# Performance work log

Hardware: AMD Instinct MI355X
Metric: run time of the kernel (lower is better)

The kernel has to match this reference:

```python
import jax, jax.numpy as jnp
import numpy as np

DIM = 1024
HEADS = 16
DIM_HEAD = 64
INNER = HEADS * DIM_HEAD  # 1024
SCALE = DIM_HEAD ** -0.5


def setup_inputs() -> dict:
    key = jax.random.key(0)
    k1, k2, k3, k4 = jax.random.split(key, 4)
    B, N = 2, 2048
    x = jax.random.normal(k1, (B, N, DIM), dtype=jnp.float32)
    # to_qkv: Linear(dim, 3*inner_dim, bias=False); weight stored as [out, in] in torch,
    # here as [in, out] for x @ W.
    w_qkv = jax.random.normal(k2, (DIM, 3 * INNER), dtype=jnp.float32) * (DIM ** -0.5)
    # to_out: Linear(inner_dim, dim) with bias
    w_out = jax.random.normal(k3, (INNER, DIM), dtype=jnp.float32) * (INNER ** -0.5)
    b_out = jax.random.normal(k4, (DIM,), dtype=jnp.float32) * 0.02
    return {"x": x, "w_qkv": w_qkv, "w_out": w_out, "b_out": b_out}


def reference(x, w_qkv, w_out, b_out):
    B, N, _ = x.shape
    qkv = x @ w_qkv                                  # [B, N, 3*INNER]
    q, k, v = jnp.split(qkv, 3, axis=-1)             # each [B, N, INNER]
    def to_heads(t):
        return t.reshape(B, N, HEADS, DIM_HEAD).transpose(0, 2, 1, 3)  # [B,H,N,D]
    q, k, v = to_heads(q), to_heads(k), to_heads(v)
    dots = jnp.einsum('bhnd,bhmd->bhnm', q, k) * SCALE  # [B,H,N,N]
    attn = jax.nn.softmax(dots, axis=-1)
    out = jnp.einsum('bhnm,bhmd->bhnd', attn, v)        # [B,H,N,D]
    out = out.transpose(0, 2, 1, 3).reshape(B, N, INNER)
    return out @ w_out + b_out
```

## Files before the change

kernel.cpp:

```cpp
#include <hip/hip_runtime.h>
#include <hip/hip_bf16.h>
#include <stdint.h>

#define PDIM   1024
#define HEADS  16
#define DHEAD  64
#define BATCH  2
#define SEQ    2048
#define ROWS   (BATCH*SEQ)
#define NBH    (BATCH*HEADS)

typedef __attribute__((ext_vector_type(8))) short s8v;
typedef __attribute__((ext_vector_type(4))) float f32x4;
typedef __attribute__((ext_vector_type(16))) float f32x16;
typedef unsigned short ushort_t;
typedef unsigned int   uint32;

#define QSCALE 0.18033688011112042f
#define MFIX 12.0f

__device__ __forceinline__ ushort_t f2bf(float x){
  union { float f; uint32 u; } v; v.f = x;
  uint32 r = v.u + 0x7FFFu + ((v.u >> 16) & 1u);
  return (ushort_t)(r >> 16);
}
__device__ __forceinline__ uint32 cvt_pk_bf16(float lo, float hi){
  uint32 r;
  asm("v_cvt_pk_bf16_f32 %0, %1, %2" : "=v"(r) : "v"(lo), "v"(hi));
  return r;
}

typedef const __attribute__((address_space(1))) void* gas_ptr;
typedef __attribute__((address_space(3))) void*       las_ptr;
__device__ __forceinline__ void g2l16(const void* g, void* l){
  __builtin_amdgcn_global_load_lds((gas_ptr)g, (las_ptr)l, 16, 0, 0);
}

__global__ __launch_bounds__(256) void k_prep(
    const float* __restrict__ x, const float* __restrict__ w_qkv,
    const float* __restrict__ w_out,
    ushort_t* __restrict__ Xh, ushort_t* __restrict__ Wqt_h,
    ushort_t* __restrict__ Wot_h){
  __shared__ float tile[64][65];
  const int bid = blockIdx.x;
  if (bid < 4096){
    int i = bid * 256 + threadIdx.x;
    float4 v = reinterpret_cast<const float4*>(x)[i];
    reinterpret_cast<ushort4*>(Xh)[i] =
        make_ushort4(f2bf(v.x), f2bf(v.y), f2bf(v.z), f2bf(v.w));
    return;
  }
  const float* src; ushort_t* dst; int R, C, cb, rb;
  float scl = 1.f;
  if (bid < 4864){
    int t = bid - 4096; src = w_qkv; dst = Wqt_h; R = 1024; C = 3072;
    cb = (t % 48) * 64; rb = (t / 48) * 64;
    if (cb < 1024) scl = QSCALE;
  } else {
    int t = bid - 4864; src = w_out; dst = Wot_h; R = 1024; C = 1024;
    cb = (t % 16) * 64; rb = (t / 16) * 64;
  }
  int t = threadIdx.x;
  int lw = t >> 6, lc = t & 63;
#pragma unroll
  for (int i = 0; i < 16; i++){
    int r = i * 4 + lw;
    tile[r][lc] = src[(size_t)(rb + r) * C + cb + lc];
  }
  __syncthreads();
#pragma unroll
  for (int i = 0; i < 16; i++){
    int c = i * 4 + lw;
    dst[(size_t)(cb + c) * R + rb + lc] = f2bf(tile[lc][c] * scl);
  }
}

#define GBM 128
#define GBN 128
#define GBK 64

__global__ __launch_bounds__(256, 2) void k_gemm_qkv(
    const ushort_t* __restrict__ Xh, const ushort_t* __restrict__ Wqt_h,
    ushort_t* __restrict__ Qh, ushort_t* __restrict__ Kh, ushort_t* __restrict__ Vth){
  __shared__ __align__(16) ushort_t Asm[2][GBM * GBK];
  __shared__ __align__(16) ushort_t Bsm[2][GBM * GBK];
  const int tid  = threadIdx.x;
  const int wave = tid >> 6, lane = tid & 63;
  const int mb = blockIdx.y * GBM, nb = blockIdx.x * GBN;
  const int wr = wave >> 1, wc = wave & 1;
  const int l15 = lane & 15, l4 = lane >> 4;
  const int rsub = lane >> 3;
  const int schunk = ((lane & 7) ^ rsub) * 8;
  f32x4 acc[4][4] = {};

  auto stage = [&](int buf, int kb){
    int k0 = kb * GBK;
#pragma unroll
    for (int i = 0; i < 4; i++){
      int row = (i * 4 + wave) * 8 + rsub;
      g2l16(Xh    + (size_t)(mb + row) * 1024 + k0 + schunk, &Asm[buf][(i * 4 + wave) * 512]);
      g2l16(Wqt_h + (size_t)(nb + row) * 1024 + k0 + schunk, &Bsm[buf][(i * 4 + wave) * 512]);
    }
  };

  stage(0, 0);

  for (int kb = 0; kb < 16; kb++){
    const int cur = kb & 1;
    if (kb < 15){
      stage(cur ^ 1, kb + 1);
      asm volatile("s_waitcnt vmcnt(8)" ::: "memory");
    } else {
      asm volatile("s_waitcnt vmcnt(0)" ::: "memory");
    }
    __builtin_amdgcn_s_barrier();
    __builtin_amdgcn_s_setprio(1);
#pragma unroll
    for (int ks = 0; ks < 2; ks++){
      s8v af[4], bfr[4];
#pragma unroll
      for (int f = 0; f < 4; f++){
        int ch = (((ks * 4 + l4) ^ (l15 & 7)) << 3);
        af[f]  = *reinterpret_cast<const s8v*>(&Asm[cur][(wr * 64 + f * 16 + l15) * 64 + ch]);
        bfr[f] = *reinterpret_cast<const s8v*>(&Bsm[cur][(wc * 64 + f * 16 + l15) * 64 + ch]);
      }
#pragma unroll
      for (int fr = 0; fr < 4; fr++)
#pragma unroll
        for (int fc = 0; fc < 4; fc++)
          acc[fr][fc] = __builtin_amdgcn_mfma_f32_16x16x32_bf16(af[fr], bfr[fc], acc[fr][fc], 0, 0, 0);
    }
    __builtin_amdgcn_s_setprio(0);
    __builtin_amdgcn_s_barrier();
  }

  const int pnum = nb >> 10;
#pragma unroll
  for (int fr = 0; fr < 4; fr++){
    int row  = mb + wr * 64 + fr * 16 + l4 * 4;
    int b    = row >> 11;
    int nseq = row & 2047;
#pragma unroll
    for (int fc = 0; fc < 4; fc++){
      int col = nb + wc * 64 + fc * 16 + l15;
      int rem = col & 1023;
      int h = rem >> 6, d = rem & 63;
      int bh = b * 16 + h;
      if (pnum == 0){
        size_t base = ((size_t)bh * SEQ + nseq) * 64 + d;
#pragma unroll
        for (int r = 0; r < 4; r++)
          Qh[base + (size_t)r * 64] = f2bf(acc[fr][fc][r]);
      } else if (pnum == 1){
        size_t base = ((size_t)bh * SEQ + nseq) * 64 + d;
#pragma unroll
        for (int r = 0; r < 4; r++)
          Kh[base + (size_t)r * 64] = f2bf(acc[fr][fc][r]);
      } else {
        size_t base = ((size_t)bh * 64 + d) * SEQ + nseq;
        *reinterpret_cast<ushort4*>(&Vth[base]) =
            make_ushort4(f2bf(acc[fr][fc][0]), f2bf(acc[fr][fc][1]),
                         f2bf(acc[fr][fc][2]), f2bf(acc[fr][fc][3]));
      }
    }
  }
}

__global__ __launch_bounds__(256, 2) void k_gemm_out(
    const ushort_t* __restrict__ Ah, const ushort_t* __restrict__ Bth,
    float* __restrict__ C, const float* __restrict__ bias){
  __shared__ __align__(16) ushort_t Asm[2][GBM * GBK];
  __shared__ __align__(16) ushort_t Bsm[2][GBM * GBK];
  const int tid  = threadIdx.x;
  const int wave = tid >> 6, lane = tid & 63;
  const int mb = blockIdx.y * GBM, nb = blockIdx.x * GBN;
  const int wr = wave >> 1, wc = wave & 1;
  const int l15 = lane & 15, l4 = lane >> 4;
  const int rsub = lane >> 3;
  const int schunk = ((lane & 7) ^ rsub) * 8;
  f32x4 acc[4][4] = {};

  auto stage = [&](int buf, int kb){
    int k0 = kb * GBK;
#pragma unroll
    for (int i = 0; i < 4; i++){
      int row = (i * 4 + wave) * 8 + rsub;
      g2l16(Ah  + (size_t)(mb + row) * 1024 + k0 + schunk, &Asm[buf][(i * 4 + wave) * 512]);
      g2l16(Bth + (size_t)(nb + row) * 1024 + k0 + schunk, &Bsm[buf][(i * 4 + wave) * 512]);
    }
  };

  stage(0, 0);

  for (int kb = 0; kb < 16; kb++){
    const int cur = kb & 1;
    if (kb < 15){
      stage(cur ^ 1, kb + 1);
      asm volatile("s_waitcnt vmcnt(8)" ::: "memory");
    } else {
      asm volatile("s_waitcnt vmcnt(0)" ::: "memory");
    }
    __builtin_amdgcn_s_barrier();
    __builtin_amdgcn_s_setprio(1);
#pragma unroll
    for (int ks = 0; ks < 2; ks++){
      s8v af[4], bfr[4];
#pragma unroll
      for (int f = 0; f < 4; f++){
        int ch = (((ks * 4 + l4) ^ (l15 & 7)) << 3);
        af[f]  = *reinterpret_cast<const s8v*>(&Asm[cur][(wr * 64 + f * 16 + l15) * 64 + ch]);
        bfr[f] = *reinterpret_cast<const s8v*>(&Bsm[cur][(wc * 64 + f * 16 + l15) * 64 + ch]);
      }
#pragma unroll
      for (int fr = 0; fr < 4; fr++)
#pragma unroll
        for (int fc = 0; fc < 4; fc++)
          acc[fr][fc] = __builtin_amdgcn_mfma_f32_16x16x32_bf16(af[fr], bfr[fc], acc[fr][fc], 0, 0, 0);
    }
    __builtin_amdgcn_s_setprio(0);
    __builtin_amdgcn_s_barrier();
  }
#pragma unroll
  for (int fr = 0; fr < 4; fr++){
    int row = mb + wr * 64 + fr * 16 + l4 * 4;
#pragma unroll
    for (int fc = 0; fc < 4; fc++){
      int col = nb + wc * 64 + fc * 16 + l15;
      float bv = bias[col];
#pragma unroll
      for (int r = 0; r < 4; r++)
        C[(size_t)(row + r) * 1024 + col] = acc[fr][fc][r] + bv;
    }
  }
}

__global__ __launch_bounds__(128, 4) void k_flash(
    const ushort_t* __restrict__ Qh, const ushort_t* __restrict__ Kh,
    const ushort_t* __restrict__ Vth, ushort_t* __restrict__ Ah){
  __shared__ __align__(16) ushort_t KhS[2][32 * 64];
  __shared__ __align__(16) ushort_t VhS[2][64 * 32];
  const int lid = blockIdx.x;
  const int xcd = lid & 7, g = lid >> 3;
  const int bh = xcd * 4 + (g & 3);
  const int qb = (g >> 2) * 64;
  const int tid = threadIdx.x, wave = tid >> 6, lane = tid & 63;
  const int l31 = lane & 31, hh = lane >> 5;
  const int b = bh >> 4, hd = bh & 15;
  const size_t hbase = (size_t)bh * SEQ * 64;
  const int rsub = lane >> 3;
  const int schunkK = ((lane & 7) ^ rsub) * 8;
  const int schunkV = ((lane & 3) ^ ((lane >> 2) & 3)) * 8;

  int fchK[4], fchV[2];
#pragma unroll
  for (int s = 0; s < 4; s++) fchK[s] = (((2 * s + hh) ^ (l31 & 7)) << 3);
#pragma unroll
  for (int s = 0; s < 2; s++) fchV[s] = (((2 * s + hh) ^ (l31 & 3)) << 3);
  const int fbK = l31 * 64;
  const int fbV = l31 * 32;

  s8v qf[4];
#pragma unroll
  for (int s = 0; s < 4; s++)
    qf[s] = *reinterpret_cast<const s8v*>(
        &Qh[hbase + (size_t)(qb + wave * 32 + l31) * 64 + s * 16 + hh * 8]);

  f32x16 o0 = {}, o1 = {};
  float lsum = 0.f;

  const ushort_t* kp0 = Kh + hbase + (size_t)(wave * 8 + rsub) * 64 + schunkK;
  const ushort_t* kp1 = kp0 + (size_t)16 * 64;
  const ushort_t* vp0 = Vth + ((size_t)bh * 64 + wave * 16 + (lane >> 2)) * SEQ + schunkV;
  const ushort_t* vp1 = vp0 + (size_t)32 * SEQ;

  auto stage = [&](int buf){
    g2l16(kp0, &KhS[buf][wave * 512]);        kp0 += 2048;
    g2l16(kp1, &KhS[buf][1024 + wave * 512]); kp1 += 2048;
    g2l16(vp0, &VhS[buf][wave * 512]);        vp0 += 32;
    g2l16(vp1, &VhS[buf][1024 + wave * 512]); vp1 += 32;
  };

  stage(0);

  for (int kt = 0; kt < 64; kt++){
    const int cur = kt & 1;
    if (kt < 63){
      stage(cur ^ 1);
      asm volatile("s_waitcnt vmcnt(4)" ::: "memory");
    } else {
      asm volatile("s_waitcnt vmcnt(0)" ::: "memory");
    }
    __builtin_amdgcn_s_barrier();

    f32x16 s0 = {};
    __builtin_amdgcn_s_setprio(1);
#pragma unroll
    for (int s = 0; s < 4; s++){
      s8v kf = *reinterpret_cast<const s8v*>(&KhS[cur][fbK + fchK[s]]);
      s0 = __builtin_amdgcn_mfma_f32_32x32x16_bf16(kf, qf[s], s0, 0, 0, 0);
    }
    __builtin_amdgcn_s_setprio(0);

    uint32 w[8];
#pragma unroll
    for (int t = 0; t < 8; t++){
      float pa = __builtin_amdgcn_exp2f(s0[2 * t]     - MFIX);
      float pb = __builtin_amdgcn_exp2f(s0[2 * t + 1] - MFIX);
      lsum += pa + pb;
      w[t] = cvt_pk_bf16(pa, pb);
    }

    __builtin_amdgcn_s_setprio(1);
#pragma unroll
    for (int s = 0; s < 2; s++){
      const int u = 4 * s;
      uint32 m0 = w[u],     m2 = w[u + 2];
      uint32 m1 = w[u + 1], m3 = w[u + 3];
      asm("v_permlane32_swap_b32 %0, %1" : "+v"(m0), "+v"(m2));
      asm("v_permlane32_swap_b32 %0, %1" : "+v"(m1), "+v"(m3));
      union { uint32 u4[4]; s8v v; } pf;
      pf.u4[0] = m0; pf.u4[1] = m1; pf.u4[2] = m2; pf.u4[3] = m3;
      s8v vf0 = *reinterpret_cast<const s8v*>(&VhS[cur][fbV + fchV[s]]);
      s8v vf1 = *reinterpret_cast<const s8v*>(&VhS[cur][fbV + 1024 + fchV[s]]);
      o0 = __builtin_amdgcn_mfma_f32_32x32x16_bf16(pf.v, vf0, o0, 0, 0, 0);
      o1 = __builtin_amdgcn_mfma_f32_32x32x16_bf16(pf.v, vf1, o1, 0, 0, 0);
    }
    __builtin_amdgcn_s_setprio(0);
    __builtin_amdgcn_s_barrier();
  }

  lsum += __shfl_xor(lsum, 32);
  float linv = 1.f / lsum;
#pragma unroll
  for (int r = 0; r < 16; r++){
    int q = (r & 3) + 8 * (r >> 2) + 4 * hh;
    float sc = __shfl(linv, q);
    int n = qb + wave * 32 + q;
    size_t rowb = (size_t)(b * SEQ + n) * 1024 + hd * 64;
    Ah[rowb + l31]      = f2bf(o0[r] * sc);
    Ah[rowb + 32 + l31] = f2bf(o1[r] * sc);
  }
}

extern "C" void kernel_launch(void* const* d_in, const int* in_sizes, int n_in,
                              void* d_out, int out_size, void* d_ws, size_t ws_size,
                              hipStream_t stream){
  const float* x     = (const float*)d_in[0];
  const float* w_qkv = (const float*)d_in[1];
  const float* w_out = (const float*)d_in[2];
  const float* b_out = (const float*)d_in[3];
  float* out = (float*)d_out;
  char* ws = (char*)d_ws;

  ushort_t* Xh    = (ushort_t*)(ws);
  ushort_t* Wqt_h = (ushort_t*)(ws + 8388608);
  ushort_t* Wot_h = (ushort_t*)(ws + 14680064);
  ushort_t* Qh    = (ushort_t*)(ws + 16777216);
  ushort_t* Kh    = (ushort_t*)(ws + 25165824);
  ushort_t* Vth   = (ushort_t*)(ws + 33554432);
  ushort_t* Ah    = (ushort_t*)(ws + 41943040);

  k_prep<<<5120, 256, 0, stream>>>(x, w_qkv, w_out, Xh, Wqt_h, Wot_h);
  k_gemm_qkv<<<dim3(24, 32), 256, 0, stream>>>(Xh, Wqt_h, Qh, Kh, Vth);
  k_flash<<<1024, 128, 0, stream>>>(Qh, Kh, Vth, Ah);
  k_gemm_out<<<dim3(8, 32), 256, 0, stream>>>(Ah, Wot_h, out, b_out);
}
```

Measured before the change: 134.0 us.

## Store K/V in MFMA fragment order and load directly to registers in flash kernel

The QKV GEMM epilogue now writes K and V in a pre-swizzled layout that matches the MFMA operand fragments of the attention kernel. The flash kernel drops LDS staging and barriers, loading each 32-key tile straight into registers with coalesced 16-byte loads, double-buffered in registers. Blocks grow to 4 waves covering 128 queries, halving the grid. This removes LDS traffic and barrier syncs, but each wave now fetches K/V on its own with no sharing through LDS, raising L2 traffic. Latency hiding now depends on register prefetch only.

```diff
diff --git a/kernel.cpp b/kernel.cpp
--- a/kernel.cpp
+++ b/kernel.cpp
@@ -81,7 +81,7 @@
 
 __global__ __launch_bounds__(256, 2) void k_gemm_qkv(
     const ushort_t* __restrict__ Xh, const ushort_t* __restrict__ Wqt_h,
-    ushort_t* __restrict__ Qh, ushort_t* __restrict__ Kh, ushort_t* __restrict__ Vth){
+    ushort_t* __restrict__ Qh, ushort_t* __restrict__ Kf, ushort_t* __restrict__ Vf){
   __shared__ __align__(16) ushort_t Asm[2][GBM * GBK];
   __shared__ __align__(16) ushort_t Bsm[2][GBM * GBK];
   const int tid  = threadIdx.x;
@@ -152,13 +152,19 @@
         for (int r = 0; r < 4; r++)
           Qh[base + (size_t)r * 64] = f2bf(acc[fr][fc][r]);
       } else if (pnum == 1){
-        size_t base = ((size_t)bh * SEQ + nseq) * 64 + d;
+        int kvt = nseq >> 5, l31p = nseq & 31;
+        int s = d >> 4, hh2 = (d >> 3) & 1, j = d & 7;
+        size_t kbase = (((size_t)bh * 64 + kvt) * 4 + s) * 512
+                     + (size_t)(hh2 * 32 + l31p) * 8 + j;
 #pragma unroll
         for (int r = 0; r < 4; r++)
-          Kh[base + (size_t)r * 64] = f2bf(acc[fr][fc][r]);
+          Kf[kbase + (size_t)r * 8] = f2bf(acc[fr][fc][r]);
       } else {
-        size_t base = ((size_t)bh * 64 + d) * SEQ + nseq;
-        *reinterpret_cast<ushort4*>(&Vth[base]) =
+        int kvt = nseq >> 5, st = (nseq >> 4) & 1, hh2 = (nseq >> 3) & 1, j0 = nseq & 7;
+        int dh = d >> 5, l31p = d & 31;
+        size_t vbase = (((size_t)bh * 64 + kvt) * 4 + st * 2 + dh) * 512
+                     + (size_t)(hh2 * 32 + l31p) * 8 + j0;
+        *reinterpret_cast<ushort4*>(&Vf[vbase]) =
             make_ushort4(f2bf(acc[fr][fc][0]), f2bf(acc[fr][fc][1]),
                          f2bf(acc[fr][fc][2]), f2bf(acc[fr][fc][3]));
       }
@@ -234,30 +240,17 @@
   }
 }
 
-__global__ __launch_bounds__(128, 4) void k_flash(
-    const ushort_t* __restrict__ Qh, const ushort_t* __restrict__ Kh,
-    const ushort_t* __restrict__ Vth, ushort_t* __restrict__ Ah){
-  __shared__ __align__(16) ushort_t KhS[2][32 * 64];
-  __shared__ __align__(16) ushort_t VhS[2][64 * 32];
+__global__ __launch_bounds__(256) void k_flash(
+    const ushort_t* __restrict__ Qh, const ushort_t* __restrict__ Kf,
+    const ushort_t* __restrict__ Vf, ushort_t* __restrict__ Ah){
   const int lid = blockIdx.x;
   const int xcd = lid & 7, g = lid >> 3;
   const int bh = xcd * 4 + (g & 3);
-  const int qb = (g >> 2) * 64;
+  const int qb = (g >> 2) * 128;
   const int tid = threadIdx.x, wave = tid >> 6, lane = tid & 63;
   const int l31 = lane & 31, hh = lane >> 5;
   const int b = bh >> 4, hd = bh & 15;
   const size_t hbase = (size_t)bh * SEQ * 64;
-  const int rsub = lane >> 3;
-  const int schunkK = ((lane & 7) ^ rsub) * 8;
-  const int schunkV = ((lane & 3) ^ ((lane >> 2) & 3)) * 8;
-
-  int fchK[4], fchV[2];
-#pragma unroll
-  for (int s = 0; s < 4; s++) fchK[s] = (((2 * s + hh) ^ (l31 & 7)) << 3);
-#pragma unroll
-  for (int s = 0; s < 2; s++) fchV[s] = (((2 * s + hh) ^ (l31 & 3)) << 3);
-  const int fbK = l31 * 64;
-  const int fbV = l31 * 32;
 
   s8v qf[4];
 #pragma unroll
@@ -265,42 +258,28 @@
     qf[s] = *reinterpret_cast<const s8v*>(
         &Qh[hbase + (size_t)(qb + wave * 32 + l31) * 64 + s * 16 + hh * 8]);
 
+  const ushort_t* kp = Kf + (size_t)bh * 64 * 2048 + lane * 8;
+  const ushort_t* vp = Vf + (size_t)bh * 64 * 2048 + lane * 8;
+
   f32x16 o0 = {}, o1 = {};
   float lsum = 0.f;
 
-  const ushort_t* kp0 = Kh + hbase + (size_t)(wave * 8 + rsub) * 64 + schunkK;
-  const ushort_t* kp1 = kp0 + (size_t)16 * 64;
-  const ushort_t* vp0 = Vth + ((size_t)bh * 64 + wave * 16 + (lane >> 2)) * SEQ + schunkV;
-  const ushort_t* vp1 = vp0 + (size_t)32 * SEQ;
-
-  auto stage = [&](int buf){
-    g2l16(kp0, &KhS[buf][wave * 512]);        kp0 += 2048;
-    g2l16(kp1, &KhS[buf][1024 + wave * 512]); kp1 += 2048;
-    g2l16(vp0, &VhS[buf][wave * 512]);        vp0 += 32;
-    g2l16(vp1, &VhS[buf][1024 + wave * 512]); vp1 += 32;
+  s8v kA[4], vA[4], kB[4], vB[4];
+
+  auto loadT = [&](s8v* k, s8v* v, int t){
+    const ushort_t* kt = kp + (size_t)t * 2048;
+    const ushort_t* vt = vp + (size_t)t * 2048;
+#pragma unroll
+    for (int s = 0; s < 4; s++) k[s] = *reinterpret_cast<const s8v*>(kt + s * 512);
+#pragma unroll
+    for (int f = 0; f < 4; f++) v[f] = *reinterpret_cast<const s8v*>(vt + f * 512);
   };
 
-  stage(0);
-
-  for (int kt = 0; kt < 64; kt++){
-    const int cur = kt & 1;
-    if (kt < 63){
-      stage(cur ^ 1);
-      asm volatile("s_waitcnt vmcnt(4)" ::: "memory");
-    } else {
-      asm volatile("s_waitcnt vmcnt(0)" ::: "memory");
-    }
-    __builtin_amdgcn_s_barrier();
-
+  auto compute = [&](const s8v* k, const s8v* v){
     f32x16 s0 = {};
-    __builtin_amdgcn_s_setprio(1);
-#pragma unroll
-    for (int s = 0; s < 4; s++){
-      s8v kf = *reinterpret_cast<const s8v*>(&KhS[cur][fbK + fchK[s]]);
-      s0 = __builtin_amdgcn_mfma_f32_32x32x16_bf16(kf, qf[s], s0, 0, 0, 0);
-    }
-    __builtin_amdgcn_s_setprio(0);
-
+#pragma unroll
+    for (int s = 0; s < 4; s++)
+      s0 = __builtin_amdgcn_mfma_f32_32x32x16_bf16(k[s], qf[s], s0, 0, 0, 0);
     uint32 w[8];
 #pragma unroll
     for (int t = 0; t < 8; t++){
@@ -309,24 +288,28 @@
       lsum += pa + pb;
       w[t] = cvt_pk_bf16(pa, pb);
     }
-
-    __builtin_amdgcn_s_setprio(1);
-#pragma unroll
-    for (int s = 0; s < 2; s++){
-      const int u = 4 * s;
+#pragma unroll
+    for (int st = 0; st < 2; st++){
+      const int u = 4 * st;
       uint32 m0 = w[u],     m2 = w[u + 2];
       uint32 m1 = w[u + 1], m3 = w[u + 3];
       asm("v_permlane32_swap_b32 %0, %1" : "+v"(m0), "+v"(m2));
       asm("v_permlane32_swap_b32 %0, %1" : "+v"(m1), "+v"(m3));
-      union { uint32 u4[4]; s8v v; } pf;
+      union { uint32 u4[4]; s8v v8; } pf;
       pf.u4[0] = m0; pf.u4[1] = m1; pf.u4[2] = m2; pf.u4[3] = m3;
-      s8v vf0 = *reinterpret_cast<const s8v*>(&VhS[cur][fbV + fchV[s]]);
-      s8v vf1 = *reinterpret_cast<const s8v*>(&VhS[cur][fbV + 1024 + fchV[s]]);
-      o0 = __builtin_amdgcn_mfma_f32_32x32x16_bf16(pf.v, vf0, o0, 0, 0, 0);
-      o1 = __builtin_amdgcn_mfma_f32_32x32x16_bf16(pf.v, vf1, o1, 0, 0, 0);
-    }
-    __builtin_amdgcn_s_setprio(0);
-    __builtin_amdgcn_s_barrier();
+      o0 = __builtin_amdgcn_mfma_f32_32x32x16_bf16(pf.v8, v[st * 2 + 0], o0, 0, 0, 0);
+      o1 = __builtin_amdgcn_mfma_f32_32x32x16_bf16(pf.v8, v[st * 2 + 1], o1, 0, 0, 0);
+    }
+  };
+
+  loadT(kA, vA, 0);
+  loadT(kB, vB, 1);
+
+  for (int t = 0; t < 64; t += 2){
+    compute(kA, vA);
+    if (t + 2 < 64) loadT(kA, vA, t + 2);
+    compute(kB, vB);
+    if (t + 3 < 64) loadT(kB, vB, t + 3);
   }
 
   lsum += __shfl_xor(lsum, 32);
@@ -356,12 +339,12 @@
   ushort_t* Wqt_h = (ushort_t*)(ws + 8388608);
   ushort_t* Wot_h = (ushort_t*)(ws + 14680064);
   ushort_t* Qh    = (ushort_t*)(ws + 16777216);
-  ushort_t* Kh    = (ushort_t*)(ws + 25165824);
-  ushort_t* Vth   = (ushort_t*)(ws + 33554432);
+  ushort_t* Kf    = (ushort_t*)(ws + 25165824);
+  ushort_t* Vf    = (ushort_t*)(ws + 33554432);
   ushort_t* Ah    = (ushort_t*)(ws + 41943040);
 
   k_prep<<<5120, 256, 0, stream>>>(x, w_qkv, w_out, Xh, Wqt_h, Wot_h);
-  k_gemm_qkv<<<dim3(24, 32), 256, 0, stream>>>(Xh, Wqt_h, Qh, Kh, Vth);
-  k_flash<<<1024, 128, 0, stream>>>(Qh, Kh, Vth, Ah);
+  k_gemm_qkv<<<dim3(24, 32), 256, 0, stream>>>(Xh, Wqt_h, Qh, Kf, Vf);
+  k_flash<<<512, 256, 0, stream>>>(Qh, Kf, Vf, Ah);
   k_gemm_out<<<dim3(8, 32), 256, 0, stream>>>(Ah, Wot_h, out, b_out);
 }
```

Measured after the change: 122.0 us. 1.1x faster.
